# Optimization experiments

Measured on AMD Instinct MI355X. Metric: run time of the kernel, lower is better.

Reference implementation:

```python
import jax, jax.numpy as jnp
import numpy as np

EPS = 1e-8  # torch F.cosine_similarity eps


def setup_inputs() -> dict:
    key = jax.random.key(0)
    ks = jax.random.split(key, 12)
    B, H, W, D, Tq = 16, 32, 32, 768, 1024
    s = 1.0 / np.sqrt(D)
    inp = {
        "image_features": jax.random.normal(ks[0], (B, H, W, D), jnp.float32),
        "text_features": jax.random.normal(ks[1], (B, Tq, D), jnp.float32),
        "image_padding_mask": jax.random.randint(ks[2], (B, H, W), 0, 2).astype(bool),
        "Wq": jax.random.normal(ks[3], (D, D), jnp.float32) * s,
        "bq": jnp.zeros((D,), jnp.float32),
        "Wk": jax.random.normal(ks[4], (D, D), jnp.float32) * s,
        "bk": jnp.zeros((D,), jnp.float32),
        "W1": jax.random.normal(ks[5], (16, 1), jnp.float32),
        "b1": jnp.zeros((16,), jnp.float32),
        "W2": jax.random.normal(ks[6], (1, 16), jnp.float32) * 0.25,
        "b2": jnp.zeros((1,), jnp.float32),
    }
    return inp


def reference(image_features, text_features, image_padding_mask,
              Wq, bq, Wk, bk, W1, b1, W2, b2):
    B, H, W_, D = image_features.shape
    # projections (torch Linear: x @ W.T + b)
    q = text_features @ Wq.T + bq                      # [B, Tq, D]
    k = (image_features @ Wk.T + bk).reshape(B, H * W_, D)  # [B, Tk, D]
    pad = image_padding_mask.reshape(B, H * W_)        # [B, Tk] True = pad
    # cosine similarity: normalize with eps-clamped norms, then dot
    qn = q / jnp.maximum(jnp.linalg.norm(q, axis=-1, keepdims=True), EPS)
    kn = k / jnp.maximum(jnp.linalg.norm(k, axis=-1, keepdims=True), EPS)
    scores = jnp.einsum('bqd,bkd->bqk', qn, kn)        # [B, Tq, Tk]
    scores = jnp.where(pad[:, None, :], -jnp.inf, scores)
    max_w = scores.max(axis=-1)                        # [B, Tq]
    # tiny MLP 1 -> 16 -> 1 with sigmoid
    h = jax.nn.relu(max_w[..., None] @ W1.T + b1)      # [B, Tq, 16]
    out = jax.nn.sigmoid(h @ W2.T + b2)[..., 0]        # [B, Tq]
    return out
```

## Files before the change

### kernel.cpp

```cpp
#include <hip/hip_runtime.h>
#include <hip/hip_bf16.h>
#include <math.h>

typedef float  f32x4 __attribute__((ext_vector_type(4)));
typedef short  s16x8 __attribute__((ext_vector_type(8)));
typedef unsigned short u16x4 __attribute__((ext_vector_type(4)));
typedef unsigned u32x4 __attribute__((ext_vector_type(4)));

__device__ __forceinline__ unsigned short f2bf(float f) {
  unsigned u = __float_as_uint(f);
  u += 0x7FFFu + ((u >> 16) & 1u);
  return (unsigned short)(u >> 16);
}
__device__ __forceinline__ u32x4 cvt8(f32x4 a, f32x4 b) {
  union { __hip_bfloat162 h; unsigned u; } c0, c1, c2, c3;
  c0.h = __float22bfloat162_rn(float2{a[0], a[1]});
  c1.h = __float22bfloat162_rn(float2{a[2], a[3]});
  c2.h = __float22bfloat162_rn(float2{b[0], b[1]});
  c3.h = __float22bfloat162_rn(float2{b[2], b[3]});
  u32x4 o; o[0] = c0.u; o[1] = c1.u; o[2] = c2.u; o[3] = c3.u;
  return o;
}
__device__ __forceinline__ unsigned fenc2(float f) {
  unsigned u = __float_as_uint(f);
  u = (u & 0x80000000u) ? ~u : (u | 0x80000000u);
  return u - 0x007FFFFFu;
}
__device__ __forceinline__ float fdec2(unsigned u) {
  u += 0x007FFFFFu;
  u = (u & 0x80000000u) ? (u & 0x7FFFFFFFu) : ~u;
  return __uint_as_float(u);
}
__device__ __forceinline__ void gload16(const void* g, void* l) {
  __builtin_amdgcn_global_load_lds(
      (const __attribute__((address_space(1))) unsigned int*)g,
      (__attribute__((address_space(3))) unsigned int*)l, 16, 0, 0);
}

__global__ __launch_bounds__(256) void cvt2w(const float* __restrict__ a,
                                             const float* __restrict__ b,
                                             unsigned short* __restrict__ da,
                                             unsigned short* __restrict__ db,
                                             unsigned* __restrict__ initzone) {
  const int n4 = 147456;
  int i = blockIdx.x * 256 + threadIdx.x;
  int stride = gridDim.x * 256;
  if (i < 49152) initzone[i] = 0;
  for (; i < 2 * n4; i += stride) {
    const float* s = (i < n4) ? a : b;
    unsigned short* d = (i < n4) ? da : db;
    int j = (i < n4) ? i : i - n4;
    f32x4 v = ((const f32x4*)s)[j];
    u16x4 o;
    o[0] = f2bf(v[0]); o[1] = f2bf(v[1]); o[2] = f2bf(v[2]); o[3] = f2bf(v[3]);
    ((u16x4*)d)[j] = o;
  }
}

__global__ __launch_bounds__(256) void proj(const float* __restrict__ Xq,
                                            const float* __restrict__ Xk,
                                            const unsigned short* __restrict__ Wqb,
                                            const unsigned short* __restrict__ Wkb,
                                            const float* __restrict__ bq,
                                            const float* __restrict__ bk,
                                            unsigned short* __restrict__ Qh,
                                            unsigned short* __restrict__ Kh,
                                            float* __restrict__ qssq,
                                            float* __restrict__ kssq) {
  const int K = 768;
  __shared__ __align__(16) unsigned short sA[128 * 64];
  __shared__ __align__(16) unsigned short sB[128 * 64];
  int id = blockIdx.x;
  int xcd = id & 7, j = id >> 3;
  int by = j % 6, bxl = j / 6;
  int bx = xcd * 16 + bxl;
  const float* A; const unsigned short* Bw; const float* bias;
  unsigned short* Out; float* ssq;
  if (blockIdx.z == 0) { A = Xq; Bw = Wqb; bias = bq; Out = Qh; ssq = qssq; }
  else                 { A = Xk; Bw = Wkb; bias = bk; Out = Kh; ssq = kssq; }

  const int t = threadIdx.x;
  const int lane = t & 63, w = t >> 6;
  const int wr = w >> 1, wc = w & 1;
  const int m0 = bx * 128, n0 = by * 128;
  const float* Ab = A + (size_t)m0 * K;
  const unsigned short* Bb = Bw + (size_t)n0 * K;
  f32x4 acc[4][4] = {};
  const int srow = t >> 3;
  const int scol = (t & 7) * 8;
  const int hsw = scol ^ ((srow & 7) << 3);
  const int lg = lane >> 4, li = lane & 15;

  for (int k0 = 0; k0 < K; k0 += 64) {
#pragma unroll
    for (int s = 0; s < 4; ++s) {
      int row = srow + s * 32;
      gload16(Bb + (size_t)row * K + k0 + hsw, (char*)sB + t * 16 + s * 4096);
    }
#pragma unroll
    for (int s = 0; s < 4; ++s) {
      int row = srow + s * 32;
      const float* src = Ab + (size_t)row * K + k0 + scol;
      f32x4 v0 = *(const f32x4*)(src);
      f32x4 v1 = *(const f32x4*)(src + 4);
      *(u32x4*)(sA + row * 64 + (scol ^ ((row & 7) << 3))) = cvt8(v0, v1);
    }
    __syncthreads();
#pragma unroll
    for (int ks = 0; ks < 2; ++ks) {
      s16x8 af[4], bfr[4];
#pragma unroll
      for (int mi = 0; mi < 4; ++mi) {
        int row = wr * 64 + mi * 16 + li;
        af[mi] = *(const s16x8*)(sA + row * 64 + ((ks * 32 + lg * 8) ^ ((row & 7) << 3)));
      }
#pragma unroll
      for (int ni = 0; ni < 4; ++ni) {
        int row = wc * 64 + ni * 16 + li;
        bfr[ni] = *(const s16x8*)(sB + row * 64 + ((ks * 32 + lg * 8) ^ ((row & 7) << 3)));
      }
#pragma unroll
      for (int mi = 0; mi < 4; ++mi)
#pragma unroll
        for (int ni = 0; ni < 4; ++ni)
          acc[mi][ni] = __builtin_amdgcn_mfma_f32_16x16x32_bf16(af[mi], bfr[ni], acc[mi][ni], 0, 0, 0);
    }
    __syncthreads();
  }
  float bv[4]; int col[4];
#pragma unroll
  for (int ni = 0; ni < 4; ++ni) { col[ni] = n0 + wc * 64 + ni * 16 + li; bv[ni] = bias[col[ni]]; }
#pragma unroll
  for (int mi = 0; mi < 4; ++mi) {
    int rbase = m0 + wr * 64 + mi * 16 + lg * 4;
#pragma unroll
    for (int r = 0; r < 4; ++r) {
      float s = 0.f;
#pragma unroll
      for (int ni = 0; ni < 4; ++ni) {
        float v = acc[mi][ni][r] + bv[ni];
        Out[(size_t)(rbase + r) * 768 + col[ni]] = f2bf(v);
        s += v * v;
      }
#pragma unroll
      for (int off = 1; off < 16; off <<= 1) s += __shfl_xor(s, off, 64);
      if (li == 0) atomicAdd(&ssq[rbase + r], s);
    }
  }
}

__global__ __launch_bounds__(256) void scores_max(const unsigned short* __restrict__ Qh,
                                                  const unsigned short* __restrict__ Kh,
                                                  const float* __restrict__ kssq,
                                                  const int* __restrict__ pad,
                                                  unsigned* __restrict__ umax) {
  const int K = 768;
  __shared__ __align__(16) unsigned short sA[128 * 64];
  __shared__ __align__(16) unsigned short sB[128 * 64];
  int id = blockIdx.x;
  int x = id & 7, g = id >> 3;
  int tile = g & 63;
  int qt = tile & 7, kt_ = tile >> 3;
  int b = ((g >> 6) << 3) | x;

  const int t = threadIdx.x;
  const int lane = t & 63, w = t >> 6;
  const int wr = w >> 1, wc = w & 1;
  const unsigned short* Ab = Qh + ((size_t)b * 1024 + qt * 128) * K;
  const unsigned short* Bb = Kh + ((size_t)b * 1024 + kt_ * 128) * K;
  f32x4 acc[4][4] = {};
  const int srow = t >> 3;
  const int scol = (t & 7) * 8;
  const int hsw = scol ^ ((srow & 7) << 3);
  const int lg = lane >> 4, li = lane & 15;

  for (int k0 = 0; k0 < K; k0 += 64) {
#pragma unroll
    for (int s = 0; s < 4; ++s) {
      int row = srow + s * 32;
      gload16(Ab + (size_t)row * K + k0 + hsw, (char*)sA + t * 16 + s * 4096);
      gload16(Bb + (size_t)row * K + k0 + hsw, (char*)sB + t * 16 + s * 4096);
    }
    __syncthreads();
#pragma unroll
    for (int ks = 0; ks < 2; ++ks) {
      s16x8 af[4], bfr[4];
#pragma unroll
      for (int mi = 0; mi < 4; ++mi) {
        int row = wr * 64 + mi * 16 + li;
        af[mi] = *(const s16x8*)(sA + row * 64 + ((ks * 32 + lg * 8) ^ ((row & 7) << 3)));
      }
#pragma unroll
      for (int ni = 0; ni < 4; ++ni) {
        int row = wc * 64 + ni * 16 + li;
        bfr[ni] = *(const s16x8*)(sB + row * 64 + ((ks * 32 + lg * 8) ^ ((row & 7) << 3)));
      }
#pragma unroll
      for (int mi = 0; mi < 4; ++mi)
#pragma unroll
        for (int ni = 0; ni < 4; ++ni)
          acc[mi][ni] = __builtin_amdgcn_mfma_f32_16x16x32_bf16(af[mi], bfr[ni], acc[mi][ni], 0, 0, 0);
    }
    __syncthreads();
  }
  float rk[4]; bool valid[4];
#pragma unroll
  for (int ni = 0; ni < 4; ++ni) {
    int gcol = b * 1024 + kt_ * 128 + wc * 64 + ni * 16 + li;
    rk[ni] = 1.0f / fmaxf(sqrtf(kssq[gcol]), 1e-8f);
    valid[ni] = (pad[gcol] == 0);
  }
#pragma unroll
  for (int mi = 0; mi < 4; ++mi) {
#pragma unroll
    for (int r = 0; r < 4; ++r) {
      float v = -INFINITY;
#pragma unroll
      for (int ni = 0; ni < 4; ++ni)
        if (valid[ni]) v = fmaxf(v, acc[mi][ni][r] * rk[ni]);
#pragma unroll
      for (int off = 1; off < 16; off <<= 1) v = fmaxf(v, __shfl_xor(v, off, 64));
      if (li == 0) {
        int row = b * 1024 + qt * 128 + wr * 64 + mi * 16 + lg * 4 + r;
        unsigned e = fenc2(v);
        if (e) atomicMax(&umax[row], e);
      }
    }
  }
}

__global__ __launch_bounds__(256) void mlp_kernel(const unsigned* __restrict__ umax,
                                                  const float* __restrict__ qssq,
                                                  const float* __restrict__ w1,
                                                  const float* __restrict__ b1,
                                                  const float* __restrict__ w2,
                                                  const float* __restrict__ b2,
                                                  float* __restrict__ out, int n) {
  int i = blockIdx.x * 256 + threadIdx.x;
  if (i >= n) return;
  float m = fdec2(umax[i]) / fmaxf(sqrtf(qssq[i]), 1e-8f);
  float s = b2[0];
#pragma unroll
  for (int j = 0; j < 16; ++j) s += w2[j] * fmaxf(m * w1[j] + b1[j], 0.f);
  out[i] = 1.f / (1.f + expf(-s));
}

extern "C" void kernel_launch(void* const* d_in, const int* in_sizes, int n_in,
                              void* d_out, int out_size, void* d_ws, size_t ws_size,
                              hipStream_t stream) {
  const float* image = (const float*)d_in[0];
  const float* text  = (const float*)d_in[1];
  const int*   pad   = (const int*)d_in[2];
  const float* Wq    = (const float*)d_in[3];
  const float* bq    = (const float*)d_in[4];
  const float* Wk    = (const float*)d_in[5];
  const float* bk    = (const float*)d_in[6];
  const float* W1    = (const float*)d_in[7];
  const float* b1    = (const float*)d_in[8];
  const float* W2    = (const float*)d_in[9];
  const float* b2    = (const float*)d_in[10];
  float* out = (float*)d_out;

  char* ws = (char*)d_ws;
  unsigned*       um  = (unsigned*)(ws);
  float*          qss = (float*)(ws + 65536);
  float*          kss = (float*)(ws + 131072);
  unsigned short* Wqb = (unsigned short*)(ws + 196608);
  unsigned short* Wkb = (unsigned short*)(ws + 1376256);
  unsigned short* Qh  = (unsigned short*)(ws + 2555904);
  unsigned short* Kh  = (unsigned short*)(ws + 27721728);

  cvt2w<<<1152, 256, 0, stream>>>(Wq, Wk, Wqb, Wkb, um);
  proj<<<dim3(768, 1, 2), 256, 0, stream>>>(text, image, Wqb, Wkb, bq, bk, Qh, Kh, qss, kss);
  scores_max<<<1024, 256, 0, stream>>>(Qh, Kh, kss, pad, um);
  mlp_kernel<<<64, 256, 0, stream>>>(um, qss, W1, b1, W2, b2, out, 16384);
}
```

Baseline: 239.9 us.

## Pipeline scores_max with 4-stage LDS ring buffer and 8 waves per block

Rewrites the scores_max GEMM main loop to prefetch three K-tiles ahead into a 4-deep shared-memory ring using async global-to-LDS loads, with explicit vmcnt waits and a single barrier per iteration. The block grows to 512 threads (8 waves, each computing 64x32), and MFMA sections are wrapped in setprio to favor matrix issue. The goal is to hide global load latency and cut barrier stalls, at the cost of 128KB of LDS, which limits the kernel to one block per CU.

```diff
diff --git a/kernel.cpp b/kernel.cpp
--- a/kernel.cpp
+++ b/kernel.cpp
@@ -149,14 +149,14 @@
   }
 }
 
-__global__ __launch_bounds__(256) void scores_max(const unsigned short* __restrict__ Qh,
-                                                  const unsigned short* __restrict__ Kh,
-                                                  const float* __restrict__ kssq,
-                                                  const int* __restrict__ pad,
-                                                  unsigned* __restrict__ umax) {
+__global__ __launch_bounds__(512, 1) void scores_max(const unsigned short* __restrict__ Qh,
+                                                     const unsigned short* __restrict__ Kh,
+                                                     const float* __restrict__ kssq,
+                                                     const int* __restrict__ pad,
+                                                     unsigned* __restrict__ umax) {
   const int K = 768;
-  __shared__ __align__(16) unsigned short sA[128 * 64];
-  __shared__ __align__(16) unsigned short sB[128 * 64];
+  __shared__ __align__(16) unsigned short sA[4][128 * 64];
+  __shared__ __align__(16) unsigned short sB[4][128 * 64];
   int id = blockIdx.x;
   int x = id & 7, g = id >> 3;
   int tile = g & 63;
@@ -165,48 +165,72 @@
 
   const int t = threadIdx.x;
   const int lane = t & 63, w = t >> 6;
-  const int wr = w >> 1, wc = w & 1;
+  const int wr = w >> 2, wcn = w & 3;
   const unsigned short* Ab = Qh + ((size_t)b * 1024 + qt * 128) * K;
   const unsigned short* Bb = Kh + ((size_t)b * 1024 + kt_ * 128) * K;
-  f32x4 acc[4][4] = {};
-  const int srow = t >> 3;
-  const int scol = (t & 7) * 8;
-  const int hsw = scol ^ ((srow & 7) << 3);
+  f32x4 acc[4][2] = {};
   const int lg = lane >> 4, li = lane & 15;
-
-  for (int k0 = 0; k0 < K; k0 += 64) {
-#pragma unroll
-    for (int s = 0; s < 4; ++s) {
-      int row = srow + s * 32;
-      gload16(Ab + (size_t)row * K + k0 + hsw, (char*)sA + t * 16 + s * 4096);
-      gload16(Bb + (size_t)row * K + k0 + hsw, (char*)sB + t * 16 + s * 4096);
-    }
-    __syncthreads();
+  const int r0 = t >> 3;
+  const int r1 = (512 + t) >> 3;
+  const int c8 = (t & 7) * 8;
+  const int sc0 = c8 ^ ((r0 & 7) << 3);
+  const int sc1 = c8 ^ ((r1 & 7) << 3);
+
+#define STAGE(KT)                                                              \
+  {                                                                            \
+    const int _s = (KT) & 3;                                                   \
+    gload16(Ab + (size_t)r0 * K + (KT) * 64 + sc0, (char*)sA[_s] + t * 16);    \
+    gload16(Ab + (size_t)r1 * K + (KT) * 64 + sc1, (char*)sA[_s] + 8192 + t * 16); \
+    gload16(Bb + (size_t)r0 * K + (KT) * 64 + sc0, (char*)sB[_s] + t * 16);    \
+    gload16(Bb + (size_t)r1 * K + (KT) * 64 + sc1, (char*)sB[_s] + 8192 + t * 16); \
+  }
+
+  STAGE(0); STAGE(1); STAGE(2);
+  asm volatile("s_waitcnt vmcnt(8)" ::: "memory");
+  __builtin_amdgcn_s_barrier();
+  __builtin_amdgcn_sched_barrier(0);
+
+#pragma unroll
+  for (int kt = 0; kt < 12; ++kt) {
+    if (kt + 3 < 12) STAGE(kt + 3);
+    __builtin_amdgcn_sched_barrier(0);
+    const unsigned short* cA = sA[kt & 3];
+    const unsigned short* cB = sB[kt & 3];
 #pragma unroll
     for (int ks = 0; ks < 2; ++ks) {
-      s16x8 af[4], bfr[4];
+      s16x8 af[4], bfr[2];
 #pragma unroll
       for (int mi = 0; mi < 4; ++mi) {
         int row = wr * 64 + mi * 16 + li;
-        af[mi] = *(const s16x8*)(sA + row * 64 + ((ks * 32 + lg * 8) ^ ((row & 7) << 3)));
-      }
-#pragma unroll
-      for (int ni = 0; ni < 4; ++ni) {
-        int row = wc * 64 + ni * 16 + li;
-        bfr[ni] = *(const s16x8*)(sB + row * 64 + ((ks * 32 + lg * 8) ^ ((row & 7) << 3)));
-      }
+        af[mi] = *(const s16x8*)(cA + row * 64 + ((ks * 32 + lg * 8) ^ ((row & 7) << 3)));
+      }
+#pragma unroll
+      for (int ni = 0; ni < 2; ++ni) {
+        int row = wcn * 32 + ni * 16 + li;
+        bfr[ni] = *(const s16x8*)(cB + row * 64 + ((ks * 32 + lg * 8) ^ ((row & 7) << 3)));
+      }
+      __builtin_amdgcn_s_setprio(1);
 #pragma unroll
       for (int mi = 0; mi < 4; ++mi)
 #pragma unroll
-        for (int ni = 0; ni < 4; ++ni)
+        for (int ni = 0; ni < 2; ++ni)
           acc[mi][ni] = __builtin_amdgcn_mfma_f32_16x16x32_bf16(af[mi], bfr[ni], acc[mi][ni], 0, 0, 0);
-    }
-    __syncthreads();
-  }
-  float rk[4]; bool valid[4];
-#pragma unroll
-  for (int ni = 0; ni < 4; ++ni) {
-    int gcol = b * 1024 + kt_ * 128 + wc * 64 + ni * 16 + li;
+      __builtin_amdgcn_s_setprio(0);
+    }
+    if (kt < 9)        asm volatile("s_waitcnt vmcnt(8)" ::: "memory");
+    else if (kt == 9)  asm volatile("s_waitcnt vmcnt(4)" ::: "memory");
+    else if (kt == 10) asm volatile("s_waitcnt vmcnt(0)" ::: "memory");
+    if (kt < 11) {
+      __builtin_amdgcn_s_barrier();
+      __builtin_amdgcn_sched_barrier(0);
+    }
+  }
+#undef STAGE
+
+  float rk[2]; bool valid[2];
+#pragma unroll
+  for (int ni = 0; ni < 2; ++ni) {
+    int gcol = b * 1024 + kt_ * 128 + wcn * 32 + ni * 16 + li;
     rk[ni] = 1.0f / fmaxf(sqrtf(kssq[gcol]), 1e-8f);
     valid[ni] = (pad[gcol] == 0);
   }
@@ -216,7 +240,7 @@
     for (int r = 0; r < 4; ++r) {
       float v = -INFINITY;
 #pragma unroll
-      for (int ni = 0; ni < 4; ++ni)
+      for (int ni = 0; ni < 2; ++ni)
         if (valid[ni]) v = fmaxf(v, acc[mi][ni][r] * rk[ni]);
 #pragma unroll
       for (int off = 1; off < 16; off <<= 1) v = fmaxf(v, __shfl_xor(v, off, 64));
@@ -272,6 +296,6 @@
 
   cvt2w<<<1152, 256, 0, stream>>>(Wq, Wk, Wqb, Wkb, um);
   proj<<<dim3(768, 1, 2), 256, 0, stream>>>(text, image, Wqb, Wkb, bq, bk, Qh, Kh, qss, kss);
-  scores_max<<<1024, 256, 0, stream>>>(Qh, Kh, kss, pad, um);
+  scores_max<<<1024, 512, 0, stream>>>(Qh, Kh, kss, pad, um);
   mlp_kernel<<<64, 256, 0, stream>>>(um, qss, W1, b1, W2, b2, out, 16384);
 }
```

After: 248.8 us. 1.04x slower.

## Prefetch next fp32 A tile into registers to overlap with MFMA compute

Applied to the files above, without the earlier changes.

Software-pipelines the projection GEMM's A-operand loads. The next K-tile of fp32 activations is loaded into registers while the current tile is converted to bf16, stored to LDS and consumed by MFMA, hiding global-load latency behind compute. The K loop is fully unrolled at 12 iterations, with explicit waitcnt, barriers and sched_barrier to control ordering. MFMA blocks run at raised wave priority via setprio. This hardcodes K=768, adds register pressure from 32 prefetch floats per thread, and depends on the manual vmcnt(8) count staying consistent with the B async loads.

```diff
diff --git a/kernel.cpp b/kernel.cpp
--- a/kernel.cpp
+++ b/kernel.cpp
@@ -91,7 +91,17 @@
   const int hsw = scol ^ ((srow & 7) << 3);
   const int lg = lane >> 4, li = lane & 15;
 
-  for (int k0 = 0; k0 < K; k0 += 64) {
+  f32x4 pa0[4], pa1[4];
+#pragma unroll
+  for (int s = 0; s < 4; ++s) {
+    const float* src = Ab + (size_t)(srow + s * 32) * K + scol;
+    pa0[s] = *(const f32x4*)src; pa1[s] = *(const f32x4*)(src + 4);
+  }
+  __builtin_amdgcn_sched_barrier(0);
+
+#pragma unroll
+  for (int kt = 0; kt < 12; ++kt) {
+    const int k0 = kt * 64;
 #pragma unroll
     for (int s = 0; s < 4; ++s) {
       int row = srow + s * 32;
@@ -100,12 +110,23 @@
 #pragma unroll
     for (int s = 0; s < 4; ++s) {
       int row = srow + s * 32;
-      const float* src = Ab + (size_t)row * K + k0 + scol;
-      f32x4 v0 = *(const f32x4*)(src);
-      f32x4 v1 = *(const f32x4*)(src + 4);
-      *(u32x4*)(sA + row * 64 + (scol ^ ((row & 7) << 3))) = cvt8(v0, v1);
-    }
-    __syncthreads();
+      *(u32x4*)(sA + row * 64 + (scol ^ ((row & 7) << 3))) = cvt8(pa0[s], pa1[s]);
+    }
+    if (kt < 11) {
+      const int k0n = k0 + 64;
+#pragma unroll
+      for (int s = 0; s < 4; ++s) {
+        const float* src = Ab + (size_t)(srow + s * 32) * K + k0n + scol;
+        pa0[s] = *(const f32x4*)src; pa1[s] = *(const f32x4*)(src + 4);
+      }
+      __builtin_amdgcn_sched_barrier(0);
+      asm volatile("s_waitcnt vmcnt(8) lgkmcnt(0)" ::: "memory");
+    } else {
+      __builtin_amdgcn_sched_barrier(0);
+      asm volatile("s_waitcnt vmcnt(0) lgkmcnt(0)" ::: "memory");
+    }
+    __builtin_amdgcn_s_barrier();
+    __builtin_amdgcn_sched_barrier(0);
 #pragma unroll
     for (int ks = 0; ks < 2; ++ks) {
       s16x8 af[4], bfr[4];
@@ -119,13 +140,17 @@
         int row = wc * 64 + ni * 16 + li;
         bfr[ni] = *(const s16x8*)(sB + row * 64 + ((ks * 32 + lg * 8) ^ ((row & 7) << 3)));
       }
+      __builtin_amdgcn_s_setprio(1);
 #pragma unroll
       for (int mi = 0; mi < 4; ++mi)
 #pragma unroll
         for (int ni = 0; ni < 4; ++ni)
           acc[mi][ni] = __builtin_amdgcn_mfma_f32_16x16x32_bf16(af[mi], bfr[ni], acc[mi][ni], 0, 0, 0);
-    }
-    __syncthreads();
+      __builtin_amdgcn_s_setprio(0);
+    }
+    asm volatile("s_waitcnt lgkmcnt(0)" ::: "memory");
+    __builtin_amdgcn_s_barrier();
+    __builtin_amdgcn_sched_barrier(0);
   }
   float bv[4]; int col[4];
 #pragma unroll
```

After: 238.7 us. Within noise of the previous version (-0.5%).
